# Kernel tuning notes

Hardware: AMD Instinct MI355X
Metric: run time of the kernel (lower is better)

The kernel has to match this reference:

```python
import jax, jax.numpy as jnp
import numpy as np

N_NODES = 50000
N_REL = 8
N_EDGES = 100000
IN_SIZE = 128
OUT_SIZE = 128


def setup_inputs() -> dict:
    key = jax.random.key(0)
    k1, k2, k3, k4, k5 = jax.random.split(key, 5)
    inp = jax.random.normal(k1, (N_NODES, IN_SIZE), dtype=jnp.float32)
    src = jax.random.randint(k2, (N_REL, N_EDGES), 0, N_NODES, dtype=jnp.int32)
    dst = jax.random.randint(k3, (N_REL, N_EDGES), 0, N_NODES, dtype=jnp.int32)
    vals = jax.random.uniform(k4, (N_REL, N_EDGES), dtype=jnp.float32)
    weights = jax.random.normal(k5, (N_REL, IN_SIZE, OUT_SIZE), dtype=jnp.float32) * (1.0 / np.sqrt(IN_SIZE))
    return {"inp": inp, "src": src, "dst": dst, "vals": vals, "weights": weights}


def reference(inp, src, dst, vals, weights):
    # Per-relation sparse adj @ inp:  agg[r] = A_r @ inp, A_r given as COO edges.
    n_nodes = inp.shape[0]

    def rel_agg(s, d, v):
        msgs = v[:, None] * inp[s]                      # [E, in]
        return jax.ops.segment_sum(msgs, d, num_segments=n_nodes)  # [N, in]

    agg = jax.vmap(rel_agg)(src, dst, vals)             # [R, N, in]
    # concat along features then block-stacked weight matmul == per-relation
    # matmul summed over relations: out = sum_r agg[r] @ W[r]
    out = jnp.einsum('rni,rio->no', agg, weights)       # [N, out]
    return out
```

## Files before the change

kernel.cpp:

```cpp
#include <hip/hip_runtime.h>


constexpr int IN  = 128;
constexpr int OUT = 128;
constexpr int LDK = 136;

typedef __attribute__((ext_vector_type(8))) short bf16x8;
typedef __attribute__((ext_vector_type(4))) float f32x4;

__device__ inline unsigned short f2bf(float f) {
    unsigned int u = __float_as_uint(f);
    u += 0x7fffu + ((u >> 16) & 1u);
    return (unsigned short)(u >> 16);
}
__device__ inline float bflo(unsigned int u) { return __uint_as_float(u << 16); }
__device__ inline float bfhi(unsigned int u) { return __uint_as_float(u & 0xffff0000u); }

__global__ __launch_bounds__(256) void conv_inp_kernel(
    const float* __restrict__ x, unsigned short* __restrict__ y, int n8)
{
    const int i = blockIdx.x * 256 + threadIdx.x;
    if (i >= n8) return;
    const float4 a = ((const float4*)x)[i * 2];
    const float4 b = ((const float4*)x)[i * 2 + 1];
    uint4 o;
    o.x = (unsigned)f2bf(a.x) | ((unsigned)f2bf(a.y) << 16);
    o.y = (unsigned)f2bf(a.z) | ((unsigned)f2bf(a.w) << 16);
    o.z = (unsigned)f2bf(b.x) | ((unsigned)f2bf(b.y) << 16);
    o.w = (unsigned)f2bf(b.z) | ((unsigned)f2bf(b.w) << 16);
    ((uint4*)y)[i] = o;
}

__global__ __launch_bounds__(256) void conv_w_kernel(
    const float* __restrict__ w, unsigned short* __restrict__ wt, int total)
{
    const int t = blockIdx.x * 256 + threadIdx.x;
    if (t >= total) return;
    const int r = t >> 14, rem = t & 16383;
    const int n = rem >> 7, k = rem & 127;
    wt[t] = f2bf(w[(r << 14) + (k << 7) + n]);
}

__global__ __launch_bounds__(256) void mfma_gemm(
    const unsigned short* __restrict__ inpb,
    const unsigned short* __restrict__ wt,
    unsigned short* __restrict__ h, int rel_base, int n_nodes)
{
    __shared__ unsigned short As[128 * LDK];

    const int rel = rel_base + blockIdx.y;
    const int row0 = blockIdx.x * 128;
    const int tid = threadIdx.x;
    const int wave = tid >> 6, lane = tid & 63;
    const int m = lane & 15, q = lane >> 4;

    {
        const int r = tid >> 1;
        const int half = (tid & 1) * 64;
        const int grow = row0 + r;
        const uint4* gp = (const uint4*)(inpb + (size_t)grow * IN + half);
        uint4* lp = (uint4*)&As[r * LDK + half];
        #pragma unroll
        for (int i = 0; i < 8; ++i) {
            uint4 v = make_uint4(0u, 0u, 0u, 0u);
            if (grow < n_nodes) v = gp[i];
            lp[i] = v;
        }
    }

    bf16x8 bfrag[2][4];
    {
        const unsigned short* wtr = wt + ((size_t)rel * OUT + wave * 32) * IN;
        #pragma unroll
        for (int nt = 0; nt < 2; ++nt)
            #pragma unroll
            for (int ks = 0; ks < 4; ++ks)
                bfrag[nt][ks] = *(const bf16x8*)(
                    wtr + (size_t)(nt * 16 + m) * IN + ks * 32 + q * 8);
    }

    __syncthreads();

    f32x4 acc[8][2];
    #pragma unroll
    for (int mt = 0; mt < 8; ++mt)
        #pragma unroll
        for (int nt = 0; nt < 2; ++nt)
            acc[mt][nt] = (f32x4){0.f, 0.f, 0.f, 0.f};

    #pragma unroll
    for (int ks = 0; ks < 4; ++ks) {
        bf16x8 a[8];
        #pragma unroll
        for (int mt = 0; mt < 8; ++mt)
            a[mt] = *(const bf16x8*)&As[(mt * 16 + m) * LDK + ks * 32 + q * 8];
        #pragma unroll
        for (int mt = 0; mt < 8; ++mt) {
            acc[mt][0] = __builtin_amdgcn_mfma_f32_16x16x32_bf16(
                a[mt], bfrag[0][ks], acc[mt][0], 0, 0, 0);
            acc[mt][1] = __builtin_amdgcn_mfma_f32_16x16x32_bf16(
                a[mt], bfrag[1][ks], acc[mt][1], 0, 0, 0);
        }
    }

    unsigned short* hrel = h + (size_t)blockIdx.y * n_nodes * OUT;
    #pragma unroll
    for (int mt = 0; mt < 8; ++mt) {
        #pragma unroll
        for (int rg = 0; rg < 4; ++rg) {
            const int row = row0 + mt * 16 + q * 4 + rg;
            if (row < n_nodes) {
                unsigned short* hp = hrel + (size_t)row * OUT + wave * 32 + m;
                hp[0]  = f2bf(acc[mt][0][rg]);
                hp[16] = f2bf(acc[mt][1][rg]);
            }
        }
    }
}

__global__ __launch_bounds__(256) void fill_kernel(
    const int* __restrict__ src, const int* __restrict__ dst,
    const float* __restrict__ vals, int* __restrict__ counts,
    int2* __restrict__ bucket, int4* __restrict__ spill,
    int* __restrict__ spill_cnt, int n_edges, int n_nodes,
    int cap, int spill_max)
{
    const int e = blockIdx.x * 256 + threadIdx.x;
    if (e >= n_edges) return;
    const size_t g = (size_t)blockIdx.y * n_edges + e;
    const int d = dst[g];
    const int enc = blockIdx.y * n_nodes + src[g];
    const int pos = atomicAdd(&counts[d], 1);
    if (pos < cap) {
        bucket[(size_t)d * cap + pos] = make_int2(enc, __float_as_int(vals[g]));
    } else {
        const int sp = atomicAdd(spill_cnt, 1);
        if (sp < spill_max)
            spill[sp] = make_int4(d, enc, __float_as_int(vals[g]), 0);
    }
}

__global__ __launch_bounds__(256) void gather_kernel(
    const unsigned short* __restrict__ h, const int2* __restrict__ bucket,
    const int* __restrict__ counts, float* __restrict__ out,
    int n_nodes, int cap, int accum)
{
    const int node = blockIdx.x * 8 + (threadIdx.x >> 5);
    const int lane = threadIdx.x & 31;
    if (node >= n_nodes) return;
    int cnt = counts[node];
    if (cnt > cap) cnt = cap;
    const int2* __restrict__ b = bucket + (size_t)node * cap;
    float4* __restrict__ op = (float4*)(out + (size_t)node * OUT);

    float4 acc = accum ? op[lane] : make_float4(0.f, 0.f, 0.f, 0.f);
    int j = 0;
    for (; j + 4 <= cnt; j += 4) {
        const int2 r0 = b[j], r1 = b[j + 1], r2 = b[j + 2], r3 = b[j + 3];
        const uint2 h0 = ((const uint2*)(h + (size_t)r0.x * OUT))[lane];
        const uint2 h1 = ((const uint2*)(h + (size_t)r1.x * OUT))[lane];
        const uint2 h2 = ((const uint2*)(h + (size_t)r2.x * OUT))[lane];
        const uint2 h3 = ((const uint2*)(h + (size_t)r3.x * OUT))[lane];
        const float v0 = __int_as_float(r0.y), v1 = __int_as_float(r1.y);
        const float v2 = __int_as_float(r2.y), v3 = __int_as_float(r3.y);
        acc.x += v0*bflo(h0.x) + v1*bflo(h1.x) + v2*bflo(h2.x) + v3*bflo(h3.x);
        acc.y += v0*bfhi(h0.x) + v1*bfhi(h1.x) + v2*bfhi(h2.x) + v3*bfhi(h3.x);
        acc.z += v0*bflo(h0.y) + v1*bflo(h1.y) + v2*bflo(h2.y) + v3*bflo(h3.y);
        acc.w += v0*bfhi(h0.y) + v1*bfhi(h1.y) + v2*bfhi(h2.y) + v3*bfhi(h3.y);
    }
    for (; j < cnt; ++j) {
        const int2 r0 = b[j];
        const float v = __int_as_float(r0.y);
        const uint2 hv = ((const uint2*)(h + (size_t)r0.x * OUT))[lane];
        acc.x += v * bflo(hv.x); acc.y += v * bfhi(hv.x);
        acc.z += v * bflo(hv.y); acc.w += v * bfhi(hv.y);
    }
    op[lane] = acc;
}

__global__ __launch_bounds__(256) void spill_kernel(
    const unsigned short* __restrict__ h, const int4* __restrict__ spill,
    const int* __restrict__ spill_cnt, float* __restrict__ out, int spill_max)
{
    int n = *spill_cnt;
    if (n > spill_max) n = spill_max;
    const int w = (blockIdx.x * 256 + threadIdx.x) >> 6;
    const int lane = threadIdx.x & 63;
    const int nw = gridDim.x * 4;
    for (int i = w; i < n; i += nw) {
        const int4 s = spill[i];
        const float v = __int_as_float(s.z);
        const unsigned int u = ((const unsigned int*)(h + (size_t)s.y * OUT))[lane];
        float* __restrict__ orow = out + (size_t)s.x * OUT;
        __hip_atomic_fetch_add(orow + lane * 2,     v * bflo(u),
                               __ATOMIC_RELAXED, __HIP_MEMORY_SCOPE_AGENT);
        __hip_atomic_fetch_add(orow + lane * 2 + 1, v * bfhi(u),
                               __ATOMIC_RELAXED, __HIP_MEMORY_SCOPE_AGENT);
    }
}

__global__ __launch_bounds__(256) void scatter_kernel(
    const unsigned short* __restrict__ h, const int* __restrict__ src,
    const int* __restrict__ dst, const float* __restrict__ vals,
    float* __restrict__ out, int n_edges)
{
    const int e = blockIdx.x * 8 + (threadIdx.x >> 5);
    if (e >= n_edges) return;
    const int lane = threadIdx.x & 31;
    const int s = src[e];
    const int d = dst[e];
    const float v = vals[e];
    const unsigned int* __restrict__ hrow =
        (const unsigned int*)(h + (size_t)s * OUT);
    float* __restrict__ orow = out + (size_t)d * OUT;
    #pragma unroll
    for (int kk = 0; kk < 2; ++kk) {
        const int jj = lane + kk * 32;
        const unsigned int u = hrow[jj];
        __hip_atomic_fetch_add(orow + jj * 2,     v * bflo(u),
                               __ATOMIC_RELAXED, __HIP_MEMORY_SCOPE_AGENT);
        __hip_atomic_fetch_add(orow + jj * 2 + 1, v * bfhi(u),
                               __ATOMIC_RELAXED, __HIP_MEMORY_SCOPE_AGENT);
    }
}

extern "C" void kernel_launch(void* const* d_in, const int* in_sizes, int n_in,
                              void* d_out, int out_size, void* d_ws, size_t ws_size,
                              hipStream_t stream) {
    const float* inp     = (const float*)d_in[0];
    const int*   src     = (const int*)  d_in[1];
    const int*   dst     = (const int*)  d_in[2];
    const float* vals    = (const float*)d_in[3];
    const float* weights = (const float*)d_in[4];
    float* out = (float*)d_out;

    const int n_nodes = in_sizes[0] / IN;
    const int n_rel   = in_sizes[4] / (IN * OUT);
    const int n_edges = in_sizes[1] / n_rel;

    auto align_up = [](size_t x) { return (x + 255) & ~(size_t)255; };
    const int SPILL_MAX = 65536;
    const size_t sz_inpb   = align_up((size_t)n_nodes * IN * 2);
    const size_t sz_wt     = align_up((size_t)n_rel * IN * OUT * 2);
    const size_t sz_counts = align_up((size_t)(n_nodes + 1) * 4);
    const size_t sz_spill  = align_up((size_t)SPILL_MAX * 16);
    const size_t fixed = sz_inpb + sz_wt + sz_counts + sz_spill;

    const int conv_n8 = n_nodes * IN / 8;
    const int wt_tot  = n_rel * IN * OUT;
    const int gemm_gx = (n_nodes + 127) / 128;
    const int gath_gx = (n_nodes + 7) / 8;
    const int fill_gx = (n_edges + 255) / 256;

    {
        const size_t sz_h = (size_t)n_rel * n_nodes * OUT * 2;
        int cap = 0;
        const int caps[] = {64, 48, 32, 24, 20};
        for (int c : caps) {
            if (fixed + sz_h + align_up((size_t)n_nodes * c * 8) <= ws_size) {
                cap = c; break;
            }
        }
        if (cap > 0) {
            char* p = (char*)d_ws;
            unsigned short* inpb = (unsigned short*)p;  p += sz_inpb;
            unsigned short* wtb  = (unsigned short*)p;  p += sz_wt;
            int*   counts = (int*)p;    p += sz_counts;
            int4*  spill  = (int4*)p;   p += sz_spill;
            unsigned short* h = (unsigned short*)p;     p += sz_h;
            int2*  bucket = (int2*)p;
            int*   spill_cnt = counts + n_nodes;

            conv_inp_kernel<<<(conv_n8 + 255) / 256, 256, 0, stream>>>(
                inp, inpb, conv_n8);
            conv_w_kernel<<<(wt_tot + 255) / 256, 256, 0, stream>>>(
                weights, wtb, wt_tot);
            hipMemsetAsync(counts, 0, (size_t)(n_nodes + 1) * 4, stream);
            dim3 fg(fill_gx, n_rel);
            fill_kernel<<<fg, 256, 0, stream>>>(src, dst, vals, counts, bucket,
                                                spill, spill_cnt, n_edges,
                                                n_nodes, cap, SPILL_MAX);
            dim3 gg(gemm_gx, n_rel);
            mfma_gemm<<<gg, 256, 0, stream>>>(inpb, wtb, h, 0, n_nodes);
            gather_kernel<<<gath_gx, 256, 0, stream>>>(h, bucket, counts, out,
                                                       n_nodes, cap, 0);
            spill_kernel<<<128, 256, 0, stream>>>(h, spill, spill_cnt, out,
                                                  SPILL_MAX);
            return;
        }
    }

    {
        const size_t sz_h = (size_t)n_nodes * OUT * 2;
        int cap = 0;
        const int caps[] = {16, 12, 8};
        for (int c : caps) {
            if (fixed + sz_h + align_up((size_t)n_nodes * c * 8) <= ws_size) {
                cap = c; break;
            }
        }
        if (cap > 0) {
            char* p = (char*)d_ws;
            unsigned short* inpb = (unsigned short*)p;  p += sz_inpb;
            unsigned short* wtb  = (unsigned short*)p;  p += sz_wt;
            int*   counts = (int*)p;    p += sz_counts;
            int4*  spill  = (int4*)p;   p += sz_spill;
            unsigned short* h = (unsigned short*)p;     p += sz_h;
            int2*  bucket = (int2*)p;
            int*   spill_cnt = counts + n_nodes;

            conv_inp_kernel<<<(conv_n8 + 255) / 256, 256, 0, stream>>>(
                inp, inpb, conv_n8);
            conv_w_kernel<<<(wt_tot + 255) / 256, 256, 0, stream>>>(
                weights, wtb, wt_tot);
            for (int r = 0; r < n_rel; ++r) {
                const size_t eoff = (size_t)r * n_edges;
                hipMemsetAsync(counts, 0, (size_t)(n_nodes + 1) * 4, stream);
                dim3 fg(fill_gx, 1);
                fill_kernel<<<fg, 256, 0, stream>>>(src + eoff, dst + eoff,
                                                    vals + eoff, counts, bucket,
                                                    spill, spill_cnt, n_edges,
                                                    n_nodes, cap, SPILL_MAX);
                dim3 gg(gemm_gx, 1);
                mfma_gemm<<<gg, 256, 0, stream>>>(inpb, wtb, h, r, n_nodes);
                gather_kernel<<<gath_gx, 256, 0, stream>>>(h, bucket, counts,
                                                           out, n_nodes, cap,
                                                           r > 0 ? 1 : 0);
                spill_kernel<<<128, 256, 0, stream>>>(h, spill, spill_cnt, out,
                                                      SPILL_MAX);
            }
            return;
        }
    }

    {
        char* p = (char*)d_ws;
        unsigned short* inpb = (unsigned short*)p;  p += sz_inpb;
        unsigned short* wtb  = (unsigned short*)p;  p += sz_wt;
        unsigned short* h = (unsigned short*)p;

        conv_inp_kernel<<<(conv_n8 + 255) / 256, 256, 0, stream>>>(
            inp, inpb, conv_n8);
        conv_w_kernel<<<(wt_tot + 255) / 256, 256, 0, stream>>>(
            weights, wtb, wt_tot);
        hipMemsetAsync(out, 0, (size_t)n_nodes * OUT * 4, stream);
        const int sgx = (n_edges + 7) / 8;
        for (int r = 0; r < n_rel; ++r) {
            const size_t eoff = (size_t)r * n_edges;
            dim3 gg(gemm_gx, 1);
            mfma_gemm<<<gg, 256, 0, stream>>>(inpb, wtb, h, r, n_nodes);
            scatter_kernel<<<sgx, 256, 0, stream>>>(h, src + eoff, dst + eoff,
                                                    vals + eoff, out, n_edges);
        }
    }
}
```

Measured before the change: 223.8 us.

## Aggregate inputs per relation via CSR before GEMM, fusing relation sum into GEMM

Reorders the computation to gather-then-transform: edges are sorted into a per-(relation,node) CSR by histogram, prefix scan and fill, then bf16 input rows are aggregated per segment, and a single GEMM loops over relations and accumulates in registers before writing fp32 output once. This replaces the per-relation GEMM over all nodes followed by an atomic or bucketed gather with spill handling, and removes the capacity-limited buckets. In exchange it adds several scan launches and a bf16 rounding of the aggregated features, and the GEMM now reads R times more A data per block.

```diff
diff --git a/kernel.cpp b/kernel.cpp
--- a/kernel.cpp
+++ b/kernel.cpp
@@ -41,126 +41,111 @@
     wt[t] = f2bf(w[(r << 14) + (k << 7) + n]);
 }
 
-__global__ __launch_bounds__(256) void mfma_gemm(
-    const unsigned short* __restrict__ inpb,
-    const unsigned short* __restrict__ wt,
-    unsigned short* __restrict__ h, int rel_base, int n_nodes)
-{
-    __shared__ unsigned short As[128 * LDK];
-
-    const int rel = rel_base + blockIdx.y;
-    const int row0 = blockIdx.x * 128;
-    const int tid = threadIdx.x;
-    const int wave = tid >> 6, lane = tid & 63;
-    const int m = lane & 15, q = lane >> 4;
-
-    {
-        const int r = tid >> 1;
-        const int half = (tid & 1) * 64;
-        const int grow = row0 + r;
-        const uint4* gp = (const uint4*)(inpb + (size_t)grow * IN + half);
-        uint4* lp = (uint4*)&As[r * LDK + half];
-        #pragma unroll
-        for (int i = 0; i < 8; ++i) {
-            uint4 v = make_uint4(0u, 0u, 0u, 0u);
-            if (grow < n_nodes) v = gp[i];
-            lp[i] = v;
-        }
-    }
-
-    bf16x8 bfrag[2][4];
-    {
-        const unsigned short* wtr = wt + ((size_t)rel * OUT + wave * 32) * IN;
-        #pragma unroll
-        for (int nt = 0; nt < 2; ++nt)
-            #pragma unroll
-            for (int ks = 0; ks < 4; ++ks)
-                bfrag[nt][ks] = *(const bf16x8*)(
-                    wtr + (size_t)(nt * 16 + m) * IN + ks * 32 + q * 8);
-    }
-
-    __syncthreads();
-
-    f32x4 acc[8][2];
-    #pragma unroll
-    for (int mt = 0; mt < 8; ++mt)
-        #pragma unroll
-        for (int nt = 0; nt < 2; ++nt)
-            acc[mt][nt] = (f32x4){0.f, 0.f, 0.f, 0.f};
-
-    #pragma unroll
-    for (int ks = 0; ks < 4; ++ks) {
-        bf16x8 a[8];
-        #pragma unroll
-        for (int mt = 0; mt < 8; ++mt)
-            a[mt] = *(const bf16x8*)&As[(mt * 16 + m) * LDK + ks * 32 + q * 8];
-        #pragma unroll
-        for (int mt = 0; mt < 8; ++mt) {
-            acc[mt][0] = __builtin_amdgcn_mfma_f32_16x16x32_bf16(
-                a[mt], bfrag[0][ks], acc[mt][0], 0, 0, 0);
-            acc[mt][1] = __builtin_amdgcn_mfma_f32_16x16x32_bf16(
-                a[mt], bfrag[1][ks], acc[mt][1], 0, 0, 0);
-        }
-    }
-
-    unsigned short* hrel = h + (size_t)blockIdx.y * n_nodes * OUT;
-    #pragma unroll
-    for (int mt = 0; mt < 8; ++mt) {
-        #pragma unroll
-        for (int rg = 0; rg < 4; ++rg) {
-            const int row = row0 + mt * 16 + q * 4 + rg;
-            if (row < n_nodes) {
-                unsigned short* hp = hrel + (size_t)row * OUT + wave * 32 + m;
-                hp[0]  = f2bf(acc[mt][0][rg]);
-                hp[16] = f2bf(acc[mt][1][rg]);
-            }
-        }
-    }
-}
-
-__global__ __launch_bounds__(256) void fill_kernel(
-    const int* __restrict__ src, const int* __restrict__ dst,
-    const float* __restrict__ vals, int* __restrict__ counts,
-    int2* __restrict__ bucket, int4* __restrict__ spill,
-    int* __restrict__ spill_cnt, int n_edges, int n_nodes,
-    int cap, int spill_max)
+__global__ __launch_bounds__(256) void hist_kernel(
+    const int* __restrict__ dst, int* __restrict__ counts,
+    int n_edges, int n_nodes)
 {
     const int e = blockIdx.x * 256 + threadIdx.x;
     if (e >= n_edges) return;
     const size_t g = (size_t)blockIdx.y * n_edges + e;
-    const int d = dst[g];
-    const int enc = blockIdx.y * n_nodes + src[g];
-    const int pos = atomicAdd(&counts[d], 1);
-    if (pos < cap) {
-        bucket[(size_t)d * cap + pos] = make_int2(enc, __float_as_int(vals[g]));
-    } else {
-        const int sp = atomicAdd(spill_cnt, 1);
-        if (sp < spill_max)
-            spill[sp] = make_int4(d, enc, __float_as_int(vals[g]), 0);
-    }
-}
-
-__global__ __launch_bounds__(256) void gather_kernel(
-    const unsigned short* __restrict__ h, const int2* __restrict__ bucket,
-    const int* __restrict__ counts, float* __restrict__ out,
-    int n_nodes, int cap, int accum)
-{
-    const int node = blockIdx.x * 8 + (threadIdx.x >> 5);
+    atomicAdd(&counts[blockIdx.y * n_nodes + dst[g]], 1);
+}
+
+__global__ __launch_bounds__(256) void scan_local_kernel(
+    const int* __restrict__ counts, int* __restrict__ offs,
+    int* __restrict__ blocksum, int S)
+{
+    __shared__ int ps[256];
+    const int tid = threadIdx.x;
+    const int base = blockIdx.x * 1024 + tid * 4;
+    int c[4];
+    #pragma unroll
+    for (int i = 0; i < 4; ++i) c[i] = (base + i < S) ? counts[base + i] : 0;
+    const int total = c[0] + c[1] + c[2] + c[3];
+    ps[tid] = total;
+    __syncthreads();
+    #pragma unroll
+    for (int d = 1; d < 256; d <<= 1) {
+        const int v = (tid >= d) ? ps[tid - d] : 0;
+        __syncthreads();
+        ps[tid] += v;
+        __syncthreads();
+    }
+    int run = ps[tid] - total;
+    #pragma unroll
+    for (int i = 0; i < 4; ++i) {
+        if (base + i < S) offs[base + i] = run;
+        run += c[i];
+    }
+    if (tid == 255) blocksum[blockIdx.x] = ps[255];
+}
+
+__global__ __launch_bounds__(256) void scan_top_kernel(
+    int* __restrict__ blocksum, int nb, int* __restrict__ offs, int S)
+{
+    __shared__ int ps[256];
+    const int tid = threadIdx.x;
+    const int chunk = (nb + 255) / 256;
+    const int lo = tid * chunk;
+    const int hi = (lo + chunk < nb) ? lo + chunk : nb;
+    int vals[8];
+    int s = 0;
+    for (int i = lo; i < hi; ++i) { vals[i - lo] = blocksum[i]; s += vals[i - lo]; }
+    ps[tid] = s;
+    __syncthreads();
+    #pragma unroll
+    for (int d = 1; d < 256; d <<= 1) {
+        const int v = (tid >= d) ? ps[tid - d] : 0;
+        __syncthreads();
+        ps[tid] += v;
+        __syncthreads();
+    }
+    int run = ps[tid] - s;
+    for (int i = lo; i < hi; ++i) { const int v = vals[i - lo]; blocksum[i] = run; run += v; }
+    if (tid == 255) offs[S] = ps[255];
+}
+
+__global__ __launch_bounds__(256) void scan_apply_kernel(
+    int* __restrict__ offs, const int* __restrict__ blocksum,
+    int* __restrict__ cursor, int S)
+{
+    const int i = blockIdx.x * 256 + threadIdx.x;
+    if (i >= S) return;
+    const int v = offs[i] + blocksum[i >> 10];
+    offs[i] = v;
+    cursor[i] = v;
+}
+
+__global__ __launch_bounds__(256) void fill_kernel(
+    const int* __restrict__ src, const int* __restrict__ dst,
+    const float* __restrict__ vals, int* __restrict__ cursor,
+    int2* __restrict__ csr, int n_edges, int n_nodes)
+{
+    const int e = blockIdx.x * 256 + threadIdx.x;
+    if (e >= n_edges) return;
+    const size_t g = (size_t)blockIdx.y * n_edges + e;
+    const int seg = blockIdx.y * n_nodes + dst[g];
+    const int pos = atomicAdd(&cursor[seg], 1);
+    csr[pos] = make_int2(src[g], __float_as_int(vals[g]));
+}
+
+__global__ __launch_bounds__(256) void gather_agg_kernel(
+    const unsigned short* __restrict__ inpb, const int2* __restrict__ csr,
+    const int* __restrict__ offs, unsigned short* __restrict__ agg, int S)
+{
+    const int seg = blockIdx.x * 8 + (threadIdx.x >> 5);
     const int lane = threadIdx.x & 31;
-    if (node >= n_nodes) return;
-    int cnt = counts[node];
-    if (cnt > cap) cnt = cap;
-    const int2* __restrict__ b = bucket + (size_t)node * cap;
-    float4* __restrict__ op = (float4*)(out + (size_t)node * OUT);
-
-    float4 acc = accum ? op[lane] : make_float4(0.f, 0.f, 0.f, 0.f);
-    int j = 0;
-    for (; j + 4 <= cnt; j += 4) {
-        const int2 r0 = b[j], r1 = b[j + 1], r2 = b[j + 2], r3 = b[j + 3];
-        const uint2 h0 = ((const uint2*)(h + (size_t)r0.x * OUT))[lane];
-        const uint2 h1 = ((const uint2*)(h + (size_t)r1.x * OUT))[lane];
-        const uint2 h2 = ((const uint2*)(h + (size_t)r2.x * OUT))[lane];
-        const uint2 h3 = ((const uint2*)(h + (size_t)r3.x * OUT))[lane];
+    if (seg >= S) return;
+    const int b = offs[seg], e = offs[seg + 1];
+
+    float4 acc = make_float4(0.f, 0.f, 0.f, 0.f);
+    int j = b;
+    for (; j + 4 <= e; j += 4) {
+        const int2 r0 = csr[j], r1 = csr[j + 1], r2 = csr[j + 2], r3 = csr[j + 3];
+        const uint2 h0 = ((const uint2*)(inpb + (size_t)r0.x * IN))[lane];
+        const uint2 h1 = ((const uint2*)(inpb + (size_t)r1.x * IN))[lane];
+        const uint2 h2 = ((const uint2*)(inpb + (size_t)r2.x * IN))[lane];
+        const uint2 h3 = ((const uint2*)(inpb + (size_t)r3.x * IN))[lane];
         const float v0 = __int_as_float(r0.y), v1 = __int_as_float(r1.y);
         const float v2 = __int_as_float(r2.y), v3 = __int_as_float(r3.y);
         acc.x += v0*bflo(h0.x) + v1*bflo(h1.x) + v2*bflo(h2.x) + v3*bflo(h3.x);
@@ -168,60 +153,124 @@
         acc.z += v0*bflo(h0.y) + v1*bflo(h1.y) + v2*bflo(h2.y) + v3*bflo(h3.y);
         acc.w += v0*bfhi(h0.y) + v1*bfhi(h1.y) + v2*bfhi(h2.y) + v3*bfhi(h3.y);
     }
-    for (; j < cnt; ++j) {
-        const int2 r0 = b[j];
+    for (; j < e; ++j) {
+        const int2 r0 = csr[j];
         const float v = __int_as_float(r0.y);
-        const uint2 hv = ((const uint2*)(h + (size_t)r0.x * OUT))[lane];
+        const uint2 hv = ((const uint2*)(inpb + (size_t)r0.x * IN))[lane];
         acc.x += v * bflo(hv.x); acc.y += v * bfhi(hv.x);
         acc.z += v * bflo(hv.y); acc.w += v * bfhi(hv.y);
     }
-    op[lane] = acc;
-}
-
-__global__ __launch_bounds__(256) void spill_kernel(
-    const unsigned short* __restrict__ h, const int4* __restrict__ spill,
-    const int* __restrict__ spill_cnt, float* __restrict__ out, int spill_max)
-{
-    int n = *spill_cnt;
-    if (n > spill_max) n = spill_max;
-    const int w = (blockIdx.x * 256 + threadIdx.x) >> 6;
+    uint2 o;
+    o.x = (unsigned)f2bf(acc.x) | ((unsigned)f2bf(acc.y) << 16);
+    o.y = (unsigned)f2bf(acc.z) | ((unsigned)f2bf(acc.w) << 16);
+    ((uint2*)(agg + (size_t)seg * IN))[lane] = o;
+}
+
+__global__ __launch_bounds__(256) void mfma_gemm(
+    const unsigned short* __restrict__ agg,
+    const unsigned short* __restrict__ wt,
+    float* __restrict__ out, int rel_base, int rel_count,
+    int n_nodes, int accum)
+{
+    __shared__ unsigned short As[128 * LDK];
+
+    const int row0 = blockIdx.x * 128;
+    const int tid = threadIdx.x;
+    const int wave = tid >> 6, lane = tid & 63;
+    const int m = lane & 15, q = lane >> 4;
+
+    f32x4 acc[8][2];
+    #pragma unroll
+    for (int mt = 0; mt < 8; ++mt)
+        #pragma unroll
+        for (int nt = 0; nt < 2; ++nt)
+            acc[mt][nt] = (f32x4){0.f, 0.f, 0.f, 0.f};
+
+    for (int r = 0; r < rel_count; ++r) {
+        __syncthreads();
+        {
+            const int rowl = tid >> 1;
+            const int half = (tid & 1) * 64;
+            const int grow = row0 + rowl;
+            const uint4* gp = (const uint4*)(
+                agg + ((size_t)r * n_nodes + grow) * IN + half);
+            uint4* lp = (uint4*)&As[rowl * LDK + half];
+            #pragma unroll
+            for (int i = 0; i < 8; ++i) {
+                uint4 v = make_uint4(0u, 0u, 0u, 0u);
+                if (grow < n_nodes) v = gp[i];
+                lp[i] = v;
+            }
+        }
+        bf16x8 bfrag[2][4];
+        {
+            const unsigned short* wtr =
+                wt + ((size_t)(rel_base + r) * OUT + wave * 32) * IN;
+            #pragma unroll
+            for (int nt = 0; nt < 2; ++nt)
+                #pragma unroll
+                for (int ks = 0; ks < 4; ++ks)
+                    bfrag[nt][ks] = *(const bf16x8*)(
+                        wtr + (size_t)(nt * 16 + m) * IN + ks * 32 + q * 8);
+        }
+        __syncthreads();
+
+        #pragma unroll
+        for (int ks = 0; ks < 4; ++ks) {
+            bf16x8 a[8];
+            #pragma unroll
+            for (int mt = 0; mt < 8; ++mt)
+                a[mt] = *(const bf16x8*)&As[(mt * 16 + m) * LDK + ks * 32 + q * 8];
+            #pragma unroll
+            for (int mt = 0; mt < 8; ++mt) {
+                acc[mt][0] = __builtin_amdgcn_mfma_f32_16x16x32_bf16(
+                    a[mt], bfrag[0][ks], acc[mt][0], 0, 0, 0);
+                acc[mt][1] = __builtin_amdgcn_mfma_f32_16x16x32_bf16(
+                    a[mt], bfrag[1][ks], acc[mt][1], 0, 0, 0);
+            }
+        }
+    }
+
+    #pragma unroll
+    for (int mt = 0; mt < 8; ++mt) {
+        #pragma unroll
+        for (int rg = 0; rg < 4; ++rg) {
+            const int row = row0 + mt * 16 + q * 4 + rg;
+            if (row < n_nodes) {
+                float* op = out + (size_t)row * OUT + wave * 32 + m;
+                float v0 = acc[mt][0][rg], v1 = acc[mt][1][rg];
+                if (accum) { v0 += op[0]; v1 += op[16]; }
+                op[0] = v0; op[16] = v1;
+            }
+        }
+    }
+}
+
+__global__ __launch_bounds__(256) void gemv_scatter_kernel(
+    const float* __restrict__ inp, const float* __restrict__ weights,
+    const int* __restrict__ src, const int* __restrict__ dst,
+    const float* __restrict__ vals, float* __restrict__ out, int n_edges)
+{
+    const int e = blockIdx.x * 4 + (threadIdx.x >> 6);
+    if (e >= n_edges) return;
     const int lane = threadIdx.x & 63;
-    const int nw = gridDim.x * 4;
-    for (int i = w; i < n; i += nw) {
-        const int4 s = spill[i];
-        const float v = __int_as_float(s.z);
-        const unsigned int u = ((const unsigned int*)(h + (size_t)s.y * OUT))[lane];
-        float* __restrict__ orow = out + (size_t)s.x * OUT;
-        __hip_atomic_fetch_add(orow + lane * 2,     v * bflo(u),
-                               __ATOMIC_RELAXED, __HIP_MEMORY_SCOPE_AGENT);
-        __hip_atomic_fetch_add(orow + lane * 2 + 1, v * bfhi(u),
-                               __ATOMIC_RELAXED, __HIP_MEMORY_SCOPE_AGENT);
-    }
-}
-
-__global__ __launch_bounds__(256) void scatter_kernel(
-    const unsigned short* __restrict__ h, const int* __restrict__ src,
-    const int* __restrict__ dst, const float* __restrict__ vals,
-    float* __restrict__ out, int n_edges)
-{
-    const int e = blockIdx.x * 8 + (threadIdx.x >> 5);
-    if (e >= n_edges) return;
-    const int lane = threadIdx.x & 31;
-    const int s = src[e];
-    const int d = dst[e];
-    const float v = vals[e];
-    const unsigned int* __restrict__ hrow =
-        (const unsigned int*)(h + (size_t)s * OUT);
-    float* __restrict__ orow = out + (size_t)d * OUT;
-    #pragma unroll
-    for (int kk = 0; kk < 2; ++kk) {
-        const int jj = lane + kk * 32;
-        const unsigned int u = hrow[jj];
-        __hip_atomic_fetch_add(orow + jj * 2,     v * bflo(u),
-                               __ATOMIC_RELAXED, __HIP_MEMORY_SCOPE_AGENT);
-        __hip_atomic_fetch_add(orow + jj * 2 + 1, v * bfhi(u),
-                               __ATOMIC_RELAXED, __HIP_MEMORY_SCOPE_AGENT);
-    }
+    const int r = blockIdx.y;
+    const size_t g = (size_t)r * n_edges + e;
+    const int s = src[g], d = dst[g];
+    const float v = vals[g];
+    const float* __restrict__ arow = inp + (size_t)s * IN;
+    const float* __restrict__ W = weights + (size_t)r * IN * OUT;
+    float a0 = 0.f, a1 = 0.f;
+    for (int k = 0; k < IN; ++k) {
+        const float av = arow[k];
+        a0 = fmaf(av, W[k * OUT + lane], a0);
+        a1 = fmaf(av, W[k * OUT + lane + 64], a1);
+    }
+    float* orow = out + (size_t)d * OUT;
+    __hip_atomic_fetch_add(orow + lane, v * a0, __ATOMIC_RELAXED,
+                           __HIP_MEMORY_SCOPE_AGENT);
+    __hip_atomic_fetch_add(orow + lane + 64, v * a1, __ATOMIC_RELAXED,
+                           __HIP_MEMORY_SCOPE_AGENT);
 }
 
 extern "C" void kernel_launch(void* const* d_in, const int* in_sizes, int n_in,
@@ -239,118 +288,74 @@
     const int n_edges = in_sizes[1] / n_rel;
 
     auto align_up = [](size_t x) { return (x + 255) & ~(size_t)255; };
-    const int SPILL_MAX = 65536;
-    const size_t sz_inpb   = align_up((size_t)n_nodes * IN * 2);
-    const size_t sz_wt     = align_up((size_t)n_rel * IN * OUT * 2);
-    const size_t sz_counts = align_up((size_t)(n_nodes + 1) * 4);
-    const size_t sz_spill  = align_up((size_t)SPILL_MAX * 16);
-    const size_t fixed = sz_inpb + sz_wt + sz_counts + sz_spill;
+    const size_t sz_inpb = align_up((size_t)n_nodes * IN * 2);
+    const size_t sz_wt   = align_up((size_t)n_rel * IN * OUT * 2);
 
     const int conv_n8 = n_nodes * IN / 8;
     const int wt_tot  = n_rel * IN * OUT;
     const int gemm_gx = (n_nodes + 127) / 128;
-    const int gath_gx = (n_nodes + 7) / 8;
-    const int fill_gx = (n_edges + 255) / 256;
-
-    {
-        const size_t sz_h = (size_t)n_rel * n_nodes * OUT * 2;
-        int cap = 0;
-        const int caps[] = {64, 48, 32, 24, 20};
-        for (int c : caps) {
-            if (fixed + sz_h + align_up((size_t)n_nodes * c * 8) <= ws_size) {
-                cap = c; break;
-            }
-        }
-        if (cap > 0) {
-            char* p = (char*)d_ws;
-            unsigned short* inpb = (unsigned short*)p;  p += sz_inpb;
-            unsigned short* wtb  = (unsigned short*)p;  p += sz_wt;
-            int*   counts = (int*)p;    p += sz_counts;
-            int4*  spill  = (int4*)p;   p += sz_spill;
-            unsigned short* h = (unsigned short*)p;     p += sz_h;
-            int2*  bucket = (int2*)p;
-            int*   spill_cnt = counts + n_nodes;
-
-            conv_inp_kernel<<<(conv_n8 + 255) / 256, 256, 0, stream>>>(
-                inp, inpb, conv_n8);
-            conv_w_kernel<<<(wt_tot + 255) / 256, 256, 0, stream>>>(
-                weights, wtb, wt_tot);
-            hipMemsetAsync(counts, 0, (size_t)(n_nodes + 1) * 4, stream);
-            dim3 fg(fill_gx, n_rel);
-            fill_kernel<<<fg, 256, 0, stream>>>(src, dst, vals, counts, bucket,
-                                                spill, spill_cnt, n_edges,
-                                                n_nodes, cap, SPILL_MAX);
-            dim3 gg(gemm_gx, n_rel);
-            mfma_gemm<<<gg, 256, 0, stream>>>(inpb, wtb, h, 0, n_nodes);
-            gather_kernel<<<gath_gx, 256, 0, stream>>>(h, bucket, counts, out,
-                                                       n_nodes, cap, 0);
-            spill_kernel<<<128, 256, 0, stream>>>(h, spill, spill_cnt, out,
-                                                  SPILL_MAX);
-            return;
-        }
-    }
-
-    {
-        const size_t sz_h = (size_t)n_nodes * OUT * 2;
-        int cap = 0;
-        const int caps[] = {16, 12, 8};
-        for (int c : caps) {
-            if (fixed + sz_h + align_up((size_t)n_nodes * c * 8) <= ws_size) {
-                cap = c; break;
-            }
-        }
-        if (cap > 0) {
-            char* p = (char*)d_ws;
-            unsigned short* inpb = (unsigned short*)p;  p += sz_inpb;
-            unsigned short* wtb  = (unsigned short*)p;  p += sz_wt;
-            int*   counts = (int*)p;    p += sz_counts;
-            int4*  spill  = (int4*)p;   p += sz_spill;
-            unsigned short* h = (unsigned short*)p;     p += sz_h;
-            int2*  bucket = (int2*)p;
-            int*   spill_cnt = counts + n_nodes;
-
-            conv_inp_kernel<<<(conv_n8 + 255) / 256, 256, 0, stream>>>(
-                inp, inpb, conv_n8);
-            conv_w_kernel<<<(wt_tot + 255) / 256, 256, 0, stream>>>(
-                weights, wtb, wt_tot);
-            for (int r = 0; r < n_rel; ++r) {
-                const size_t eoff = (size_t)r * n_edges;
-                hipMemsetAsync(counts, 0, (size_t)(n_nodes + 1) * 4, stream);
-                dim3 fg(fill_gx, 1);
-                fill_kernel<<<fg, 256, 0, stream>>>(src + eoff, dst + eoff,
-                                                    vals + eoff, counts, bucket,
-                                                    spill, spill_cnt, n_edges,
-                                                    n_nodes, cap, SPILL_MAX);
-                dim3 gg(gemm_gx, 1);
-                mfma_gemm<<<gg, 256, 0, stream>>>(inpb, wtb, h, r, n_nodes);
-                gather_kernel<<<gath_gx, 256, 0, stream>>>(h, bucket, counts,
-                                                           out, n_nodes, cap,
-                                                           r > 0 ? 1 : 0);
-                spill_kernel<<<128, 256, 0, stream>>>(h, spill, spill_cnt, out,
-                                                      SPILL_MAX);
-            }
-            return;
-        }
-    }
-
-    {
+    const int edge_gx = (n_edges + 255) / 256;
+
+    for (int nr = n_rel; nr >= 1; nr = (nr == 1) ? 0 : nr / 2) {
+        const int S = nr * n_nodes;
+        const int nb = (S + 1023) / 1024;
+        const size_t sz_counts = align_up((size_t)S * 4);
+        const size_t sz_offs   = align_up((size_t)(S + 1) * 4);
+        const size_t sz_cursor = align_up((size_t)S * 4);
+        const size_t sz_bsum   = align_up((size_t)nb * 4);
+        const size_t sz_csr    = align_up((size_t)nr * n_edges * 8);
+        const size_t sz_agg    = (size_t)S * IN * 2;
+        const size_t need = sz_inpb + sz_wt + sz_counts + sz_offs + sz_cursor
+                          + sz_bsum + sz_csr + sz_agg;
+        if (need > ws_size) continue;
+
         char* p = (char*)d_ws;
         unsigned short* inpb = (unsigned short*)p;  p += sz_inpb;
         unsigned short* wtb  = (unsigned short*)p;  p += sz_wt;
-        unsigned short* h = (unsigned short*)p;
+        int*  counts = (int*)p;   p += sz_counts;
+        int*  offs   = (int*)p;   p += sz_offs;
+        int*  cursor = (int*)p;   p += sz_cursor;
+        int*  bsum   = (int*)p;   p += sz_bsum;
+        int2* csr    = (int2*)p;  p += sz_csr;
+        unsigned short* agg = (unsigned short*)p;
 
         conv_inp_kernel<<<(conv_n8 + 255) / 256, 256, 0, stream>>>(
             inp, inpb, conv_n8);
         conv_w_kernel<<<(wt_tot + 255) / 256, 256, 0, stream>>>(
             weights, wtb, wt_tot);
-        hipMemsetAsync(out, 0, (size_t)n_nodes * OUT * 4, stream);
-        const int sgx = (n_edges + 7) / 8;
-        for (int r = 0; r < n_rel; ++r) {
-            const size_t eoff = (size_t)r * n_edges;
-            dim3 gg(gemm_gx, 1);
-            mfma_gemm<<<gg, 256, 0, stream>>>(inpb, wtb, h, r, n_nodes);
-            scatter_kernel<<<sgx, 256, 0, stream>>>(h, src + eoff, dst + eoff,
-                                                    vals + eoff, out, n_edges);
-        }
-    }
-}
+
+        for (int rb = 0; rb < n_rel; rb += nr) {
+            const int rc = (rb + nr <= n_rel) ? nr : (n_rel - rb);
+            const int Sc = rc * n_nodes;
+            const int nbc = (Sc + 1023) / 1024;
+            const size_t eoff = (size_t)rb * n_edges;
+
+            hipMemsetAsync(counts, 0, (size_t)Sc * 4, stream);
+            {
+                dim3 g(edge_gx, rc);
+                hist_kernel<<<g, 256, 0, stream>>>(dst + eoff, counts,
+                                                   n_edges, n_nodes);
+            }
+            scan_local_kernel<<<nbc, 256, 0, stream>>>(counts, offs, bsum, Sc);
+            scan_top_kernel<<<1, 256, 0, stream>>>(bsum, nbc, offs, Sc);
+            scan_apply_kernel<<<(Sc + 255) / 256, 256, 0, stream>>>(
+                offs, bsum, cursor, Sc);
+            {
+                dim3 g(edge_gx, rc);
+                fill_kernel<<<g, 256, 0, stream>>>(src + eoff, dst + eoff,
+                                                   vals + eoff, cursor, csr,
+                                                   n_edges, n_nodes);
+            }
+            gather_agg_kernel<<<(Sc + 7) / 8, 256, 0, stream>>>(
+                inpb, csr, offs, agg, Sc);
+            mfma_gemm<<<gemm_gx, 256, 0, stream>>>(
+                agg, wtb, out, rb, rc, n_nodes, rb > 0 ? 1 : 0);
+        }
+        return;
+    }
+
+    hipMemsetAsync(out, 0, (size_t)n_nodes * OUT * 4, stream);
+    dim3 g((n_edges + 3) / 4, n_rel);
+    gemv_scatter_kernel<<<g, 256, 0, stream>>>(inp, weights, src, dst, vals,
+                                               out, n_edges);
+}
```

Measured after the change: 281.5 us. 25.8% more time.
